# Optimization experiments

Measured on AMD Instinct MI355X. Metric: run time of the kernel, lower is better.

## Reference

```python
import jax, jax.numpy as jnp
import numpy as np

B, C, H, W = 2, 64, 96, 96
C8 = C // 8

def _conv1x1(x, w, b):
    # x: [B, Cin, H, W], w: [Cout, Cin], b: [Cout]
    return jnp.einsum('oi,bihw->bohw', w, x) + b[None, :, None, None]

def setup_inputs() -> dict:
    key = jax.random.key(0)
    ks = jax.random.split(key, 10)
    s = lambda fan_in: 1.0 / np.sqrt(fan_in)
    return {
        'feature_maps': jax.random.normal(ks[0], (B, C, H, W), jnp.float32),
        'depth': jax.random.normal(ks[1], (B, 1, H, W), jnp.float32),
        'wa': jax.random.normal(ks[2], (C, 1), jnp.float32) * s(1),
        'ba': jax.random.normal(ks[3], (C,), jnp.float32) * s(1),
        'wb': jax.random.normal(ks[4], (C8, C), jnp.float32) * s(C),
        'bb': jax.random.normal(ks[5], (C8,), jnp.float32) * s(C),
        'wc': jax.random.normal(ks[6], (C8, C), jnp.float32) * s(C),
        'bc': jax.random.normal(ks[7], (C8,), jnp.float32) * s(C),
        'wd': jax.random.normal(ks[8], (C, C), jnp.float32) * s(C),
        'bd': jax.random.normal(ks[9], (C,), jnp.float32) * s(C),
    }

def reference(feature_maps, depth, wa, ba, wb, bb, wc, bc, wd, bd):
    b, c, h, w = feature_maps.shape
    n = h * w
    depth_feat = jax.nn.relu(_conv1x1(depth, wa, ba))          # [B,C,H,W]
    feat_b = _conv1x1(feature_maps, wb, bb).reshape(b, -1, n)  # [B,C/8,N]
    feat_b = jnp.transpose(feat_b, (0, 2, 1))                  # [B,N,C/8]
    feat_c = _conv1x1(depth_feat, wc, bc).reshape(b, -1, n)    # [B,C/8,N]
    attn = jax.nn.softmax(jnp.einsum('bnk,bkm->bnm', feat_b, feat_c), axis=-1)  # [B,N,N]
    feat_d = _conv1x1(depth_feat, wd, bd).reshape(b, -1, n)    # [B,C,N]
    # bmm(feat_d, attn^T): out[b,c,n] = sum_m feat_d[b,c,m] * attn[b,n,m]
    feat_e = jnp.einsum('bcm,bnm->bcn', feat_d, attn)
    return feat_e.reshape(b, c, h, w)
```

## Files before the change

### kernel.cpp

```cpp
#include <hip/hip_runtime.h>


#define BN 2
#define CC 64
#define C8K 8
#define NN 9216
#define SPLIT 4
#define MCHUNK 128
#define MRANGE (NN / SPLIT)
#define TQ 64
#define NBLK (NN / TQ)
#define PSTR 136

typedef __attribute__((ext_vector_type(8))) short short8;
typedef __attribute__((ext_vector_type(4))) float f32x4;

#define OFF_QB 0
#define OFF_KT (OFF_QB + BN * NN * C8K / 2)
#define OFF_VT (OFF_KT + BN * NN * C8K / 2)
#define OFF_PACC (OFF_VT + BN * NN * CC / 2)
#define OFF_PSUM (OFF_PACC + SPLIT * BN * NN * CC)
#define WS_FLOATS (OFF_PSUM + SPLIT * BN * NN)

static __device__ inline unsigned short f2bf(float x) {
    unsigned u = __builtin_bit_cast(unsigned, x);
    unsigned r = (u + 0x7fff + ((u >> 16) & 1)) >> 16;
    return (unsigned short)r;
}

__global__ __launch_bounds__(256) void pam_prep(
    const float* __restrict__ fm, const float* __restrict__ depth,
    const float* __restrict__ wa, const float* __restrict__ ba,
    const float* __restrict__ wb, const float* __restrict__ bb,
    const float* __restrict__ wc, const float* __restrict__ bc,
    const float* __restrict__ wd, const float* __restrict__ bd,
    unsigned short* __restrict__ Qb, unsigned short* __restrict__ Kt,
    unsigned short* __restrict__ Vt)
{
    __shared__ float s_wd[CC * CC];
    __shared__ float s_wb[C8K * CC], s_wc[C8K * CC];
    __shared__ float s_wa[CC], s_ba[CC], s_bd[CC];
    __shared__ float s_bb[C8K], s_bc[C8K];
    __shared__ float qp[4][TQ][C8K + 1];

    int t = threadIdx.x;
    for (int i = t; i < CC * CC; i += 256) s_wd[i] = wd[i];
    for (int i = t; i < C8K * CC; i += 256) { s_wb[i] = wb[i]; s_wc[i] = wc[i]; }
    if (t < CC) { s_wa[t] = wa[t]; s_ba[t] = ba[t]; s_bd[t] = bd[t]; }
    if (t < C8K) { s_bb[t] = bb[t]; s_bc[t] = bc[t]; }
    __syncthreads();

    int px0 = blockIdx.x * TQ;
    int b = px0 / NN;
    int m0 = px0 - b * NN;
    int px = t & 63, w = t >> 6;
    int m = m0 + px;
    int gidx = px0 + px;

    float d = depth[gidx];
    float df[CC];
#pragma unroll
    for (int i = 0; i < CC; ++i) df[i] = fmaxf(s_wa[i] * d + s_ba[i], 0.0f);

#pragma unroll 4
    for (int cc = 0; cc < 16; ++cc) {
        int c = w * 16 + cc;
        float acc = s_bd[c];
#pragma unroll
        for (int i = 0; i < CC; i += 4) {
            float4 wv = *(const float4*)&s_wd[c * CC + i];
            acc += wv.x * df[i] + wv.y * df[i + 1] + wv.z * df[i + 2] + wv.w * df[i + 3];
        }
        Vt[(b * CC + c) * NN + m] = f2bf(acc);
    }

    {
        float k0 = s_bc[2 * w], k1 = s_bc[2 * w + 1];
#pragma unroll
        for (int i = 0; i < CC; ++i) {
            k0 += s_wc[(2 * w) * CC + i] * df[i];
            k1 += s_wc[(2 * w + 1) * CC + i] * df[i];
        }
        unsigned pk = (unsigned)f2bf(k0) | ((unsigned)f2bf(k1) << 16);
        *(unsigned*)&Kt[(b * NN + m) * C8K + 2 * w] = pk;
    }

    {
        float q[C8K];
#pragma unroll
        for (int k = 0; k < C8K; ++k) q[k] = (w == 0) ? s_bb[k] : 0.0f;
#pragma unroll
        for (int ii = 0; ii < 16; ++ii) {
            int i = w * 16 + ii;
            float f = fm[(b * CC + i) * NN + m];
#pragma unroll
            for (int k = 0; k < C8K; ++k) q[k] += s_wb[k * CC + i] * f;
        }
#pragma unroll
        for (int k = 0; k < C8K; ++k) qp[w][px][k] = q[k];
    }
    __syncthreads();
    {
        int px2 = t >> 2, k2 = (t & 3) * 2;
        float a0 = qp[0][px2][k2] + qp[1][px2][k2] + qp[2][px2][k2] + qp[3][px2][k2];
        float a1 = qp[0][px2][k2 + 1] + qp[1][px2][k2 + 1] + qp[2][px2][k2 + 1] + qp[3][px2][k2 + 1];
        unsigned pk = (unsigned)f2bf(a0) | ((unsigned)f2bf(a1) << 16);
        *(unsigned*)&Qb[(px0 + px2) * C8K + k2] = pk;
    }
}

__global__ __launch_bounds__(256, 4) void pam_attn(
    const unsigned short* __restrict__ Qb, const unsigned short* __restrict__ Kt,
    const unsigned short* __restrict__ Vt,
    float* __restrict__ PACC, float* __restrict__ PSUM)
{
    __shared__ unsigned short p_s[TQ * PSTR];
    __shared__ unsigned short v_s[CC * PSTR];
    __shared__ unsigned short k_s[MCHUNK * C8K];

    int t = threadIdx.x;
    int n0 = blockIdx.x * TQ;
    int split = blockIdx.y;
    int b = blockIdx.z;
    int m_start = split * MRANGE;

    int lane = t & 63, w = t >> 6;
    int col16 = lane & 15, quad = lane >> 4;
    int vc = t >> 2, vseg = t & 3;

    const f32x4 z4 = {0.0f, 0.0f, 0.0f, 0.0f};

    short8 aq = {0, 0, 0, 0, 0, 0, 0, 0};
    if (quad == 0)
        aq = *(const short8*)&Qb[(b * NN + n0 + w * 16 + col16) * C8K];

    f32x4 acc0 = z4, acc1 = z4, acc2 = z4, acc3 = z4;
    float rsum[4] = {0.0f, 0.0f, 0.0f, 0.0f};

    const unsigned short* pA = &p_s[(w * 16 + col16) * PSTR + quad * 8];
    const unsigned short* pB = &v_s[col16 * PSTR + quad * 8];

    for (int ch = 0; ch < MRANGE; ch += MCHUNK) {
        int m0 = m_start + ch;
        __syncthreads();
        {
            const uint4* src = (const uint4*)&Vt[(b * CC + vc) * NN + m0 + vseg * 32];
            uint4* dst = (uint4*)&v_s[vc * PSTR + vseg * 32];
#pragma unroll
            for (int i = 0; i < 4; ++i) dst[i] = src[i];
        }
        if (t < MCHUNK)
            *(uint4*)&k_s[t * C8K] = *(const uint4*)&Kt[(b * NN + m0 + t) * C8K];
        __syncthreads();

        f32x4 sacc[8];
#pragma unroll
        for (int mt = 0; mt < 8; ++mt) {
            short8 bk = *(const short8*)&k_s[(mt * 16 + col16) * C8K];
            sacc[mt] = __builtin_amdgcn_mfma_f32_16x16x32_bf16(aq, bk, z4, 0, 0, 0);
        }
#pragma unroll
        for (int mt = 0; mt < 8; ++mt) {
#pragma unroll
            for (int r = 0; r < 4; ++r) {
                float e = __expf(sacc[mt][r]);
                rsum[r] += e;
                p_s[(w * 16 + quad * 4 + r) * PSTR + mt * 16 + col16] = f2bf(e);
            }
        }
#pragma unroll
        for (int kk = 0; kk < 4; ++kk) {
            short8 a = *(const short8*)(pA + kk * 32);
            short8 b0 = *(const short8*)(pB + 0 * 16 * PSTR + kk * 32);
            short8 b1 = *(const short8*)(pB + 1 * 16 * PSTR + kk * 32);
            short8 b2 = *(const short8*)(pB + 2 * 16 * PSTR + kk * 32);
            short8 b3 = *(const short8*)(pB + 3 * 16 * PSTR + kk * 32);
            acc0 = __builtin_amdgcn_mfma_f32_16x16x32_bf16(a, b0, acc0, 0, 0, 0);
            acc1 = __builtin_amdgcn_mfma_f32_16x16x32_bf16(a, b1, acc1, 0, 0, 0);
            acc2 = __builtin_amdgcn_mfma_f32_16x16x32_bf16(a, b2, acc2, 0, 0, 0);
            acc3 = __builtin_amdgcn_mfma_f32_16x16x32_bf16(a, b3, acc3, 0, 0, 0);
        }
    }

    int slab = (split * BN + b) * NN;
#pragma unroll
    for (int r = 0; r < 4; ++r) {
        float v = rsum[r];
        v += __shfl_xor(v, 1); v += __shfl_xor(v, 2);
        v += __shfl_xor(v, 4); v += __shfl_xor(v, 8);
        rsum[r] = v;
    }
    if (col16 == 0) {
#pragma unroll
        for (int r = 0; r < 4; ++r)
            PSUM[slab + n0 + w * 16 + quad * 4 + r] = rsum[r];
    }
    {
        float* base = &PACC[(slab + n0 + w * 16) * CC];
#pragma unroll
        for (int reg = 0; reg < 4; ++reg) {
            int r = quad * 4 + reg;
            base[r * CC + 0 * 16 + col16] = acc0[reg];
            base[r * CC + 1 * 16 + col16] = acc1[reg];
            base[r * CC + 2 * 16 + col16] = acc2[reg];
            base[r * CC + 3 * 16 + col16] = acc3[reg];
        }
    }
}

__global__ __launch_bounds__(256) void pam_norm(
    const float* __restrict__ PACC, const float* __restrict__ PSUM,
    float* __restrict__ out)
{
    __shared__ float tile[TQ * (CC + 1)];
    __shared__ float sums[TQ];
    int t = threadIdx.x;
    int n0 = blockIdx.x * TQ;
    int b = blockIdx.y;
    if (t < TQ) {
        float s = 0.0f;
#pragma unroll
        for (int sp = 0; sp < SPLIT; ++sp) s += PSUM[(sp * BN + b) * NN + n0 + t];
        sums[t] = s;
    }
    __syncthreads();
    int lane = t & 63, wv = t >> 6;
    for (int rr = wv * 16; rr < wv * 16 + 16; ++rr) {
        float a = 0.0f;
#pragma unroll
        for (int sp = 0; sp < SPLIT; ++sp)
            a += PACC[((sp * BN + b) * NN + n0 + rr) * CC + lane];
        tile[rr * (CC + 1) + lane] = a / sums[rr];
    }
    __syncthreads();
    for (int i = t; i < CC * TQ; i += 256) {
        int chn = i >> 6, nn2 = i & 63;
        out[(b * CC + chn) * NN + n0 + nn2] = tile[nn2 * (CC + 1) + chn];
    }
}

extern "C" void kernel_launch(void* const* d_in, const int* in_sizes, int n_in,
                              void* d_out, int out_size, void* d_ws, size_t ws_size,
                              hipStream_t stream) {
    const float* fm    = (const float*)d_in[0];
    const float* depth = (const float*)d_in[1];
    const float* wa    = (const float*)d_in[2];
    const float* ba    = (const float*)d_in[3];
    const float* wb    = (const float*)d_in[4];
    const float* bb    = (const float*)d_in[5];
    const float* wc    = (const float*)d_in[6];
    const float* bc    = (const float*)d_in[7];
    const float* wd    = (const float*)d_in[8];
    const float* bd    = (const float*)d_in[9];
    float* out = (float*)d_out;

    float* ws = (float*)d_ws;
    unsigned short* Qb = (unsigned short*)(ws + OFF_QB);
    unsigned short* Kt = (unsigned short*)(ws + OFF_KT);
    unsigned short* Vt = (unsigned short*)(ws + OFF_VT);
    float* PACC = ws + OFF_PACC;
    float* PSUM = ws + OFF_PSUM;

    pam_prep<<<dim3((BN * NN) / TQ), 256, 0, stream>>>(
        fm, depth, wa, ba, wb, bb, wc, bc, wd, bd, Qb, Kt, Vt);
    pam_attn<<<dim3(NBLK, SPLIT, BN), 256, 0, stream>>>(Qb, Kt, Vt, PACC, PSUM);
    pam_norm<<<dim3(NBLK, BN), 256, 0, stream>>>(PACC, PSUM, out);
}
```

Baseline: 172.9 us.

## Switch attention to 32x32x16 MFMA with 128-query tiles and DPP-packed P stores

Rewrites the attention kernel around 32x32x16 bf16 MFMA. Each wave now handles 32 queries, the block tile grows to 128 queries and the key chunk shrinks to 96. Exponentials are shifted by a constant, and adjacent-lane bf16 values are packed through DPP so P is written to LDS as 32-bit stores. The normalization kernel now uses float4 loads and a reciprocal multiply. Risks: the fixed shift is not a true row max and could overflow for other inputs, and occupancy drops to 3 blocks.

Result: slower. 184.6 us (+6.8%).

```diff
diff --git a/kernel.cpp b/kernel.cpp
--- a/kernel.cpp
+++ b/kernel.cpp
@@ -6,14 +6,16 @@
 #define C8K 8
 #define NN 9216
 #define SPLIT 4
-#define MCHUNK 128
+#define MCHUNK 96
 #define MRANGE (NN / SPLIT)
-#define TQ 64
-#define NBLK (NN / TQ)
-#define PSTR 136
+#define TQ 128
+#define NBLKQ (NN / TQ)
+#define PREP_PX 64
+#define SHIFT 12.0f
+#define PSTR 104
 
 typedef __attribute__((ext_vector_type(8))) short short8;
-typedef __attribute__((ext_vector_type(4))) float f32x4;
+typedef __attribute__((ext_vector_type(16))) float f32x16;
 
 #define OFF_QB 0
 #define OFF_KT (OFF_QB + BN * NN * C8K / 2)
@@ -22,10 +24,9 @@
 #define OFF_PSUM (OFF_PACC + SPLIT * BN * NN * CC)
 #define WS_FLOATS (OFF_PSUM + SPLIT * BN * NN)
 
-static __device__ inline unsigned short f2bf(float x) {
+static __device__ inline unsigned f2bf(float x) {
     unsigned u = __builtin_bit_cast(unsigned, x);
-    unsigned r = (u + 0x7fff + ((u >> 16) & 1)) >> 16;
-    return (unsigned short)r;
+    return (u + 0x7fff + ((u >> 16) & 1)) >> 16;
 }
 
 __global__ __launch_bounds__(256) void pam_prep(
@@ -41,7 +42,7 @@
     __shared__ float s_wb[C8K * CC], s_wc[C8K * CC];
     __shared__ float s_wa[CC], s_ba[CC], s_bd[CC];
     __shared__ float s_bb[C8K], s_bc[C8K];
-    __shared__ float qp[4][TQ][C8K + 1];
+    __shared__ float qp[4][PREP_PX][C8K + 1];
 
     int t = threadIdx.x;
     for (int i = t; i < CC * CC; i += 256) s_wd[i] = wd[i];
@@ -50,7 +51,7 @@
     if (t < C8K) { s_bb[t] = bb[t]; s_bc[t] = bc[t]; }
     __syncthreads();
 
-    int px0 = blockIdx.x * TQ;
+    int px0 = blockIdx.x * PREP_PX;
     int b = px0 / NN;
     int m0 = px0 - b * NN;
     int px = t & 63, w = t >> 6;
@@ -71,7 +72,7 @@
             float4 wv = *(const float4*)&s_wd[c * CC + i];
             acc += wv.x * df[i] + wv.y * df[i + 1] + wv.z * df[i + 2] + wv.w * df[i + 3];
         }
-        Vt[(b * CC + c) * NN + m] = f2bf(acc);
+        Vt[(b * CC + c) * NN + m] = (unsigned short)f2bf(acc);
     }
 
     {
@@ -81,7 +82,7 @@
             k0 += s_wc[(2 * w) * CC + i] * df[i];
             k1 += s_wc[(2 * w + 1) * CC + i] * df[i];
         }
-        unsigned pk = (unsigned)f2bf(k0) | ((unsigned)f2bf(k1) << 16);
+        unsigned pk = f2bf(k0) | (f2bf(k1) << 16);
         *(unsigned*)&Kt[(b * NN + m) * C8K + 2 * w] = pk;
     }
 
@@ -104,12 +105,12 @@
         int px2 = t >> 2, k2 = (t & 3) * 2;
         float a0 = qp[0][px2][k2] + qp[1][px2][k2] + qp[2][px2][k2] + qp[3][px2][k2];
         float a1 = qp[0][px2][k2 + 1] + qp[1][px2][k2 + 1] + qp[2][px2][k2 + 1] + qp[3][px2][k2 + 1];
-        unsigned pk = (unsigned)f2bf(a0) | ((unsigned)f2bf(a1) << 16);
+        unsigned pk = f2bf(a0) | (f2bf(a1) << 16);
         *(unsigned*)&Qb[(px0 + px2) * C8K + k2] = pk;
     }
 }
 
-__global__ __launch_bounds__(256, 4) void pam_attn(
+__global__ __launch_bounds__(256, 3) void pam_attn(
     const unsigned short* __restrict__ Qb, const unsigned short* __restrict__ Kt,
     const unsigned short* __restrict__ Vt,
     float* __restrict__ PACC, float* __restrict__ PSUM)
@@ -125,85 +126,74 @@
     int m_start = split * MRANGE;
 
     int lane = t & 63, w = t >> 6;
-    int col16 = lane & 15, quad = lane >> 4;
-    int vc = t >> 2, vseg = t & 3;
-
-    const f32x4 z4 = {0.0f, 0.0f, 0.0f, 0.0f};
-
-    short8 aq = {0, 0, 0, 0, 0, 0, 0, 0};
-    if (quad == 0)
-        aq = *(const short8*)&Qb[(b * NN + n0 + w * 16 + col16) * C8K];
-
-    f32x4 acc0 = z4, acc1 = z4, acc2 = z4, acc3 = z4;
-    float rsum[4] = {0.0f, 0.0f, 0.0f, 0.0f};
-
-    const unsigned short* pA = &p_s[(w * 16 + col16) * PSTR + quad * 8];
-    const unsigned short* pB = &v_s[col16 * PSTR + quad * 8];
+    int l31 = lane & 31, half = lane >> 5;
+
+    short8 aq = {};
+    if (lane < 32)
+        aq = *(const short8*)&Qb[(b * NN + n0 + w * 32 + l31) * C8K];
+
+    f32x16 acc0 = {}, acc1 = {};
+    float rsum[16] = {};
 
     for (int ch = 0; ch < MRANGE; ch += MCHUNK) {
         int m0 = m_start + ch;
         __syncthreads();
         {
-            const uint4* src = (const uint4*)&Vt[(b * CC + vc) * NN + m0 + vseg * 32];
-            uint4* dst = (uint4*)&v_s[vc * PSTR + vseg * 32];
-#pragma unroll
-            for (int i = 0; i < 4; ++i) dst[i] = src[i];
+            int row = t >> 2, seg = t & 3;
+            const unsigned short* gsrc = &Vt[(b * CC + row) * NN + m0 + seg * 8];
+            unsigned short* ldst = &v_s[row * PSTR + seg * 8];
+#pragma unroll
+            for (int i = 0; i < 3; ++i)
+                *(uint4*)(ldst + i * 32) = *(const uint4*)(gsrc + i * 32);
         }
         if (t < MCHUNK)
             *(uint4*)&k_s[t * C8K] = *(const uint4*)&Kt[(b * NN + m0 + t) * C8K];
         __syncthreads();
 
-        f32x4 sacc[8];
-#pragma unroll
-        for (int mt = 0; mt < 8; ++mt) {
-            short8 bk = *(const short8*)&k_s[(mt * 16 + col16) * C8K];
-            sacc[mt] = __builtin_amdgcn_mfma_f32_16x16x32_bf16(aq, bk, z4, 0, 0, 0);
-        }
-#pragma unroll
-        for (int mt = 0; mt < 8; ++mt) {
-#pragma unroll
-            for (int r = 0; r < 4; ++r) {
-                float e = __expf(sacc[mt][r]);
-                rsum[r] += e;
-                p_s[(w * 16 + quad * 4 + r) * PSTR + mt * 16 + col16] = f2bf(e);
+#pragma unroll
+        for (int mt = 0; mt < 3; ++mt) {
+            short8 bk = *(const short8*)&k_s[(mt * 32 + l31) * C8K];
+            f32x16 s = __builtin_amdgcn_mfma_f32_32x32x16_bf16(aq, bk, (f32x16){}, 0, 0, 0);
+#pragma unroll
+            for (int reg = 0; reg < 16; ++reg) {
+                float e = __expf(s[reg] - SHIFT);
+                rsum[reg] += e;
+                unsigned hb = f2bf(e);
+                unsigned other = __builtin_amdgcn_mov_dpp(hb, 0xB1, 0xF, 0xF, true);
+                if (!(lane & 1)) {
+                    int prow = w * 32 + (reg & 3) + 8 * (reg >> 2) + 4 * half;
+                    *(unsigned*)&p_s[prow * PSTR + mt * 32 + l31] = hb | (other << 16);
+                }
             }
         }
 #pragma unroll
-        for (int kk = 0; kk < 4; ++kk) {
-            short8 a = *(const short8*)(pA + kk * 32);
-            short8 b0 = *(const short8*)(pB + 0 * 16 * PSTR + kk * 32);
-            short8 b1 = *(const short8*)(pB + 1 * 16 * PSTR + kk * 32);
-            short8 b2 = *(const short8*)(pB + 2 * 16 * PSTR + kk * 32);
-            short8 b3 = *(const short8*)(pB + 3 * 16 * PSTR + kk * 32);
-            acc0 = __builtin_amdgcn_mfma_f32_16x16x32_bf16(a, b0, acc0, 0, 0, 0);
-            acc1 = __builtin_amdgcn_mfma_f32_16x16x32_bf16(a, b1, acc1, 0, 0, 0);
-            acc2 = __builtin_amdgcn_mfma_f32_16x16x32_bf16(a, b2, acc2, 0, 0, 0);
-            acc3 = __builtin_amdgcn_mfma_f32_16x16x32_bf16(a, b3, acc3, 0, 0, 0);
+        for (int ks = 0; ks < 6; ++ks) {
+            const int off = ks * 16 + half * 8;
+            short8 a  = *(const short8*)&p_s[(w * 32 + l31) * PSTR + off];
+            short8 b0 = *(const short8*)&v_s[l31 * PSTR + off];
+            short8 b1 = *(const short8*)&v_s[(32 + l31) * PSTR + off];
+            acc0 = __builtin_amdgcn_mfma_f32_32x32x16_bf16(a, b0, acc0, 0, 0, 0);
+            acc1 = __builtin_amdgcn_mfma_f32_32x32x16_bf16(a, b1, acc1, 0, 0, 0);
         }
     }
 
     int slab = (split * BN + b) * NN;
 #pragma unroll
-    for (int r = 0; r < 4; ++r) {
-        float v = rsum[r];
-        v += __shfl_xor(v, 1); v += __shfl_xor(v, 2);
-        v += __shfl_xor(v, 4); v += __shfl_xor(v, 8);
-        rsum[r] = v;
-    }
-    if (col16 == 0) {
-#pragma unroll
-        for (int r = 0; r < 4; ++r)
-            PSUM[slab + n0 + w * 16 + quad * 4 + r] = rsum[r];
-    }
-    {
-        float* base = &PACC[(slab + n0 + w * 16) * CC];
-#pragma unroll
-        for (int reg = 0; reg < 4; ++reg) {
-            int r = quad * 4 + reg;
-            base[r * CC + 0 * 16 + col16] = acc0[reg];
-            base[r * CC + 1 * 16 + col16] = acc1[reg];
-            base[r * CC + 2 * 16 + col16] = acc2[reg];
-            base[r * CC + 3 * 16 + col16] = acc3[reg];
+    for (int reg = 0; reg < 16; ++reg) {
+        float v = rsum[reg];
+        v += __shfl_xor(v, 1);  v += __shfl_xor(v, 2);
+        v += __shfl_xor(v, 4);  v += __shfl_xor(v, 8);
+        v += __shfl_xor(v, 16);
+        if (l31 == reg)
+            PSUM[slab + n0 + w * 32 + (reg & 3) + 8 * (reg >> 2) + 4 * half] = v;
+    }
+    {
+        float* base = &PACC[(slab + n0 + w * 32) * CC];
+#pragma unroll
+        for (int reg = 0; reg < 16; ++reg) {
+            int r = (reg & 3) + 8 * (reg >> 2) + 4 * half;
+            base[r * CC + l31] = acc0[reg];
+            base[r * CC + 32 + l31] = acc1[reg];
         }
     }
 }
@@ -212,30 +202,38 @@
     const float* __restrict__ PACC, const float* __restrict__ PSUM,
     float* __restrict__ out)
 {
-    __shared__ float tile[TQ * (CC + 1)];
-    __shared__ float sums[TQ];
+    __shared__ float tile[64 * 68];
+    __shared__ float sums[64];
     int t = threadIdx.x;
-    int n0 = blockIdx.x * TQ;
+    int n0 = blockIdx.x * 64;
     int b = blockIdx.y;
-    if (t < TQ) {
+    if (t < 64) {
         float s = 0.0f;
 #pragma unroll
         for (int sp = 0; sp < SPLIT; ++sp) s += PSUM[(sp * BN + b) * NN + n0 + t];
         sums[t] = s;
     }
     __syncthreads();
-    int lane = t & 63, wv = t >> 6;
-    for (int rr = wv * 16; rr < wv * 16 + 16; ++rr) {
-        float a = 0.0f;
-#pragma unroll
-        for (int sp = 0; sp < SPLIT; ++sp)
-            a += PACC[((sp * BN + b) * NN + n0 + rr) * CC + lane];
-        tile[rr * (CC + 1) + lane] = a / sums[rr];
-    }
-    __syncthreads();
-    for (int i = t; i < CC * TQ; i += 256) {
-        int chn = i >> 6, nn2 = i & 63;
-        out[(b * CC + chn) * NN + n0 + nn2] = tile[nn2 * (CC + 1) + chn];
+#pragma unroll
+    for (int it = 0; it < 4; ++it) {
+        int idx = it * 256 + t;
+        int r = idx >> 4, c4 = (idx & 15) * 4;
+        float4 a = {0.f, 0.f, 0.f, 0.f};
+#pragma unroll
+        for (int sp = 0; sp < SPLIT; ++sp) {
+            float4 p = *(const float4*)&PACC[((sp * BN + b) * NN + n0 + r) * CC + c4];
+            a.x += p.x; a.y += p.y; a.z += p.z; a.w += p.w;
+        }
+        float inv = 1.0f / sums[r];
+        a.x *= inv; a.y *= inv; a.z *= inv; a.w *= inv;
+        *(float4*)&tile[r * 68 + c4] = a;
+    }
+    __syncthreads();
+#pragma unroll
+    for (int it = 0; it < 16; ++it) {
+        int i = it * 256 + t;
+        int c = i >> 6, nn = i & 63;
+        out[(b * CC + c) * NN + n0 + nn] = tile[nn * 68 + c];
     }
 }
 
@@ -261,8 +259,8 @@
     float* PACC = ws + OFF_PACC;
     float* PSUM = ws + OFF_PSUM;
 
-    pam_prep<<<dim3((BN * NN) / TQ), 256, 0, stream>>>(
+    pam_prep<<<dim3((BN * NN) / PREP_PX), 256, 0, stream>>>(
         fm, depth, wa, ba, wb, bb, wc, bc, wd, bd, Qb, Kt, Vt);
-    pam_attn<<<dim3(NBLK, SPLIT, BN), 256, 0, stream>>>(Qb, Kt, Vt, PACC, PSUM);
-    pam_norm<<<dim3(NBLK, BN), 256, 0, stream>>>(PACC, PSUM, out);
-}
+    pam_attn<<<dim3(NBLKQ, SPLIT, BN), 256, 0, stream>>>(Qb, Kt, Vt, PACC, PSUM);
+    pam_norm<<<dim3(NN / 64, BN), 256, 0, stream>>>(PACC, PSUM, out);
+}
```
